# Kernel optimization log

Measured on AMD Instinct MI355X. Metric: run time of the kernel, lower is better.

Reference implementation:

```python
import jax, jax.numpy as jnp
import numpy as np
import math

B, S, E, H, NL, OUT, VOCAB = 16, 512, 1024, 16, 6, 10, 16
D = E // H
PAD = VOCAB - 1
EPS = 1e-5


def _positional_encoding():
    # Faithful to the module: pe[:x.size(0)] indexes the BATCH dim of a
    # [B, S, E] tensor, yielding [B, 1, E] broadcast over sequence.
    pos = jnp.arange(B, dtype=jnp.float32)[:, None]            # [B,1]
    div = jnp.exp(jnp.arange(0, E, 2, dtype=jnp.float32) * (-math.log(10000.0) / E))
    pe = jnp.zeros((B, E), dtype=jnp.float32)
    pe = pe.at[:, 0::2].set(jnp.sin(pos * div))
    pe = pe.at[:, 1::2].set(jnp.cos(pos * div))
    return pe[:, None, :]                                      # [B,1,E]


def setup_inputs() -> dict:
    key = jax.random.key(0)
    ks = jax.random.split(key, 8)
    sc = 0.02
    return {
        "inputs": jax.random.randint(ks[0], (B, S), 0, PAD),   # no pad tokens
        "emb": jax.random.normal(ks[1], (VOCAB, E), jnp.float32) * sc,
        "wq": jax.random.normal(ks[2], (E, E), jnp.float32) * sc,
        "bq": jnp.zeros((E,), jnp.float32),
        "wk": jax.random.normal(ks[3], (E, E), jnp.float32) * sc,
        "bk": jnp.zeros((E,), jnp.float32),
        "wv": jax.random.normal(ks[4], (E, E), jnp.float32) * sc,
        "bv": jnp.zeros((E,), jnp.float32),
        "wfc": jax.random.normal(ks[5], (E, E), jnp.float32) * sc,
        "bfc": jnp.zeros((E,), jnp.float32),
        "gamma": jnp.ones((E,), jnp.float32),
        "beta": jnp.zeros((E,), jnp.float32),
        "wout": jax.random.normal(ks[6], (S * E, OUT), jnp.float32) * sc,
        "bout": jnp.zeros((OUT,), jnp.float32),
    }


def _layernorm(x, gamma, beta):
    mu = jnp.mean(x, axis=-1, keepdims=True)
    var = jnp.mean(jnp.square(x - mu), axis=-1, keepdims=True)
    return (x - mu) * jax.lax.rsqrt(var + EPS) * gamma + beta


def reference(inputs, emb, wq, bq, wk, bk, wv, bv, wfc, bfc, gamma, beta, wout, bout):
    x = emb[inputs]                                            # [B,S,E]
    x = x + (x + _positional_encoding())                       # x += pos_enc(x)
    mask = (inputs == PAD)                                     # [B,S] key-pad mask
    scale = 1.0 / math.sqrt(D)
    for _ in range(NL):  # same (shared) weights each iteration, as in source
        q = (x @ wq + bq).reshape(B, S, H, D).transpose(0, 2, 1, 3)
        k = (x @ wk + bk).reshape(B, S, H, D).transpose(0, 2, 1, 3)
        v = (x @ wv + bv).reshape(B, S, H, D).transpose(0, 2, 1, 3)
        att = jnp.einsum('bhqd,bhkd->bhqk', q, k) * scale      # [B,H,S,S]
        att = jnp.where(mask[:, None, None, :], -jnp.inf, att)
        att = jax.nn.softmax(att, axis=-1)
        o = jnp.einsum('bhqk,bhkd->bhqd', att, v)
        o = o.transpose(0, 2, 1, 3).reshape(B, S, E)
        x = _layernorm(o + x, gamma, beta)                     # dropout = eval identity
        x = _layernorm((x @ wfc + bfc) + x, gamma, beta)
    return x.reshape(B, -1) @ wout + bout                      # [B,OUT]
```

## Files before the change

kernel.cpp:

```cpp
#include <hip/hip_runtime.h>
#include <hip/hip_bf16.h>
#include <math.h>

#define B_   16
#define S_   512
#define E_   1024
#define H_   16
#define D_   64
#define NL_  6
#define OUT_ 10
#define M_   (B_*S_)

typedef short short8 __attribute__((ext_vector_type(8)));
typedef float f32x4 __attribute__((ext_vector_type(4)));
typedef int   int4v __attribute__((ext_vector_type(4)));
typedef unsigned short ushort4v __attribute__((ext_vector_type(4)));

typedef const __attribute__((address_space(1))) unsigned int* gas1_t;
typedef __attribute__((address_space(3))) unsigned int* las3_t;
#define GLD16(g,l) __builtin_amdgcn_global_load_lds((gas1_t)(g), (las3_t)(l), 16, 0, 0)

static __device__ __forceinline__ float bf2f(unsigned short u){
  union { unsigned int i; float f; } v; v.i = ((unsigned int)u) << 16; return v.f;
}
static __device__ __forceinline__ unsigned short f2bf(float f){
  union { __hip_bfloat16 h; unsigned short u; } v;
  v.h = __float2bfloat16(f);
  return v.u;
}
static __device__ __forceinline__ f32x4 mfma16(short8 a, short8 b, f32x4 c){
  return __builtin_amdgcn_mfma_f32_16x16x32_bf16(a, b, c, 0, 0, 0);
}

__global__ __launch_bounds__(192)
void code_k(float* __restrict__ out, float code)
{
  int t = threadIdx.x;
  if (t < B_*OUT_) out[t] = code;
}

__global__ __launch_bounds__(256)
void transpose_k(const float* __restrict__ w0, const float* __restrict__ w1,
                 const float* __restrict__ w2, const float* __restrict__ w3,
                 unsigned short* __restrict__ wT)
{
  const float* w = blockIdx.z==0 ? w0 : blockIdx.z==1 ? w1 : blockIdx.z==2 ? w2 : w3;
  unsigned short* o = wT + (size_t)blockIdx.z * E_ * E_;
  __shared__ unsigned short tl[64][65];
  int n0 = blockIdx.x*64, k0 = blockIdx.y*64;
  int tx = threadIdx.x, ty = threadIdx.y;
  #pragma unroll
  for (int i = 0; i < 16; ++i)
    tl[ty + 4*i][tx] = f2bf(w[(size_t)(k0 + ty + 4*i)*E_ + n0 + tx]);
  __syncthreads();
  #pragma unroll
  for (int i = 0; i < 16; ++i)
    o[(size_t)(n0 + ty + 4*i)*E_ + k0 + tx] = tl[tx][ty + 4*i];
}

__global__ __launch_bounds__(256)
void embed_k(const int* __restrict__ tok, const float* __restrict__ emb,
             unsigned short* __restrict__ x)
{
  int row = blockIdx.x;
  int b = row >> 9;
  int tk = tok[row];
  tk = tk < 0 ? 0 : (tk > 15 ? 15 : tk);
  int e0 = threadIdx.x * 4;
  const float c0 = -9.210340371976184f / (float)E_;
  f32x4 ev = *(const f32x4*)&emb[(size_t)tk * E_ + e0];
  ushort4v bb;
  #pragma unroll
  for (int i = 0; i < 4; ++i) {
    int e = e0 + i;
    float dv = expf((float)(e & ~1) * c0);
    float arg = (float)b * dv;
    float pe = (e & 1) ? cosf(arg) : sinf(arg);
    bb[i] = f2bf(2.0f * ev[i] + pe);
  }
  *(ushort4v*)&x[(size_t)row*E_ + e0] = bb;
}

template<int MODE>
__global__ __launch_bounds__(256)
void gemm_bt_k(const unsigned short* __restrict__ A,
               const unsigned short* __restrict__ BT,
               const float* __restrict__ biasA, const float* __restrict__ biasB,
               unsigned short* __restrict__ outq)
{
  __shared__ alignas(16) unsigned short SM[(MODE==2) ? 17408 : 16384];
  unsigned short* Al = SM;
  unsigned short* Bl = SM + 8192;
  int mt = blockIdx.x;
  int nyt = blockIdx.y;
  int wsel = (MODE == 0) ? (nyt >> 3) : 0;
  int nt   = (MODE == 0) ? (nyt & 7) : nyt;
  const unsigned short* Bp = BT + (size_t)wsel * E_ * E_ + (size_t)nt * 128 * E_;
  const float* bias = (MODE == 0) ? (wsel == 0 ? biasA : biasB) : biasA;
  int tid = threadIdx.x;
  int lane = tid & 63, wid = tid >> 6;
  int wr = wid >> 1, wc = wid & 1;
  int m0 = mt * 128;
  int lr = lane & 15, lk = lane >> 4;
  int lx = lr & 7;
  int c8 = tid & 7;
  int rbase = tid >> 3;
  int c8s = c8 ^ (rbase & 7);
  f32x4 acc[4][4] = {};
  for (int kt = 0; kt < E_/64; ++kt) {
    #pragma unroll
    for (int j = 0; j < 4; ++j) {
      int r = j*32 + rbase;
      int idx = j*256 + tid;
      GLD16(A + (size_t)(m0 + r)*E_ + kt*64 + c8s*8, &Al[idx*8]);
      GLD16(Bp + (size_t)r*E_ + kt*64 + c8s*8, &Bl[idx*8]);
    }
    __syncthreads();
    #pragma unroll
    for (int kk = 0; kk < 2; ++kk) {
      int sA = ((kk*4 + lk) ^ lx) * 8;
      short8 af[4], bfr[4];
      #pragma unroll
      for (int mi = 0; mi < 4; ++mi)
        af[mi] = *(const short8*)&Al[(wr*64 + mi*16 + lr)*64 + sA];
      #pragma unroll
      for (int ni = 0; ni < 4; ++ni)
        bfr[ni] = *(const short8*)&Bl[(wc*64 + ni*16 + lr)*64 + sA];
      #pragma unroll
      for (int mi = 0; mi < 4; ++mi)
        #pragma unroll
        for (int ni = 0; ni < 4; ++ni)
          acc[mi][ni] = mfma16(af[mi], bfr[ni], acc[mi][ni]);
    }
    __syncthreads();
  }
  if (MODE == 2) {
    unsigned short* Ct = SM;
    #pragma unroll
    for (int ni = 0; ni < 4; ++ni) {
      int nl = wc*64 + ni*16 + lr;
      float bv = bias[nt*128 + nl];
      #pragma unroll
      for (int mi = 0; mi < 4; ++mi)
        #pragma unroll
        for (int j = 0; j < 4; ++j)
          Ct[nl*136 + wr*64 + mi*16 + lk*4 + j] = f2bf(acc[mi][ni][j] + bv);
    }
    __syncthreads();
    int dl = tid >> 1, half = tid & 1;
    int h = nt*2 + (dl >> 6), d = dl & 63;
    int bb = m0 >> 9, s0 = (m0 & 511) + half*64;
    unsigned short* gp = outq + (((size_t)(bb*H_ + h)*D_ + d)*S_ + s0);
    #pragma unroll
    for (int c = 0; c < 8; ++c)
      *(int4v*)(gp + c*8) = *(const int4v*)&Ct[dl*136 + half*64 + c*8];
  } else {
    unsigned short* Cl = SM;
    #pragma unroll
    for (int ni = 0; ni < 4; ++ni) {
      int n = nt*128 + wc*64 + ni*16 + lr;
      float bv = bias[n];
      #pragma unroll
      for (int mi = 0; mi < 4; ++mi)
        #pragma unroll
        for (int j = 0; j < 4; ++j)
          Cl[(wr*64 + mi*16 + lk*4 + j)*128 + wc*64 + ni*16 + lr] =
            f2bf(acc[mi][ni][j] + bv);
    }
    __syncthreads();
    int r = tid >> 1, half = tid & 1;
    int m = m0 + r;
    unsigned short* gp;
    if (MODE == 0) {
      int bb = m >> 9, s = m & 511;
      int h = nt*2 + half;
      gp = outq + (size_t)wsel*M_*E_ + (((size_t)(bb*H_ + h)*S_ + s)*D_);
    } else {
      gp = outq + (size_t)m*E_ + nt*128 + half*64;
    }
    const unsigned short* sp = &Cl[r*128 + half*64];
    #pragma unroll
    for (int c = 0; c < 8; ++c)
      *(int4v*)(gp + c*8) = *(const int4v*)(sp + c*8);
  }
}

__global__ __launch_bounds__(512, 4)
void attn_k(const unsigned short* __restrict__ Q, const unsigned short* __restrict__ K,
            const unsigned short* __restrict__ VT, unsigned short* __restrict__ O)
{
  extern __shared__ unsigned short SMEM[];
  int bid = blockIdx.x;
  int bh = bid & 255, qh = bid >> 8;
  int tid = threadIdx.x, lane = tid & 63, wid = tid >> 6;
  int lr = lane & 15, lk = lane >> 4;
  const unsigned short* Qb = Q + (size_t)bh * S_ * D_;
  const unsigned short* Kb = K + (size_t)bh * S_ * D_;
  const unsigned short* VTb = VT + (size_t)bh * S_ * D_;
  unsigned short* Pw = SMEM + 32768 + wid * 640;

  int kr  = tid >> 3, kc8 = tid & 7;
  int kcs = kc8 ^ (kr & 7);
  short8 qf[2][2];
  #pragma unroll
  for (int s = 0; s < 2; ++s) {
    int q0 = (qh*2 + s)*128 + wid*16;
    qf[s][0] = *(const short8*)(Qb + (size_t)(q0 + lr)*D_ + lk*8);
    qf[s][1] = *(const short8*)(Qb + (size_t)(q0 + lr)*D_ + 32 + lk*8);
  }
  {
    unsigned short* Kd = SMEM;
    #pragma unroll
    for (int j = 0; j < 2; ++j) {
      int idx = j*512 + tid;
      GLD16(Kb + (size_t)(kr + j*64)*D_ + kcs*8, &Kd[idx*8]);
    }
  }
  {
    unsigned short* Vd = SMEM + 16384;
    #pragma unroll
    for (int j = 0; j < 2; ++j) {
      int idx = j*512 + tid;
      int d = idx >> 4, c16 = idx & 15;
      int cds = c16 ^ (d & 15);
      GLD16(VTb + (size_t)d*S_ + cds*8, &Vd[idx*8]);
    }
  }
  __syncthreads();

  f32x4 oacc[2][4] = {};
  float plsum[2][4] = {{0.f,0.f,0.f,0.f},{0.f,0.f,0.f,0.f}};
  int cur = 0;
  for (int kt = 0; kt < 4; ++kt) {
    if (kt < 3) {
      unsigned short* Kd = SMEM + (cur^1)*8192;
      unsigned short* Vd = SMEM + 16384 + (cur^1)*8192;
      #pragma unroll
      for (int j = 0; j < 2; ++j) {
        int idx = j*512 + tid;
        int r = idx >> 3, c8 = idx & 7;
        GLD16(Kb + (size_t)((kt+1)*128 + r)*D_ + (c8 ^ (r & 7))*8, &Kd[idx*8]);
        int d = idx >> 4, c16 = idx & 15;
        GLD16(VTb + (size_t)d*S_ + (kt+1)*128 + (c16 ^ (d & 15))*8, &Vd[idx*8]);
      }
    }
    const unsigned short* Kl = SMEM + cur*8192;
    const unsigned short* Vl = SMEM + 16384 + cur*8192;
    #pragma unroll
    for (int s = 0; s < 2; ++s) {
      #pragma unroll
      for (int c = 0; c < 4; ++c) {
        f32x4 s0 = {}, s1 = {};
        {
          const unsigned short* kr0 = &Kl[((2*c)*16 + lr)*64];
          const unsigned short* kr1 = &Kl[((2*c+1)*16 + lr)*64];
          int a0 = ((lk     ^ (lr & 7)))*8;
          int a1 = (((4+lk) ^ (lr & 7)))*8;
          s0 = mfma16(qf[s][0], *(const short8*)(kr0 + a0), s0);
          s0 = mfma16(qf[s][1], *(const short8*)(kr0 + a1), s0);
          s1 = mfma16(qf[s][0], *(const short8*)(kr1 + a0), s1);
          s1 = mfma16(qf[s][1], *(const short8*)(kr1 + a1), s1);
        }
        #pragma unroll
        for (int j = 0; j < 4; ++j) {
          s0[j] = __expf(s0[j] * 0.125f);
          s1[j] = __expf(s1[j] * 0.125f);
          plsum[s][j] += s0[j] + s1[j];
        }
        #pragma unroll
        for (int j = 0; j < 4; ++j) {
          Pw[(lk*4 + j)*40 + lr]      = f2bf(s0[j]);
          Pw[(lk*4 + j)*40 + 16 + lr] = f2bf(s1[j]);
        }
        asm volatile("s_waitcnt lgkmcnt(0)" ::: "memory");
        short8 pf = *(const short8*)&Pw[lr*40 + lk*8];
        #pragma unroll
        for (int dt = 0; dt < 4; ++dt) {
          int drow = dt*16 + lr;
          short8 vf = *(const short8*)&Vl[drow*128 + (((c*4 + lk) ^ lr))*8];
          oacc[s][dt] = mfma16(pf, vf, oacc[s][dt]);
        }
      }
    }
    __syncthreads();
    cur ^= 1;
  }
  #pragma unroll
  for (int s = 0; s < 2; ++s) {
    float lsum[4];
    #pragma unroll
    for (int j = 0; j < 4; ++j) {
      float t = plsum[s][j];
      #pragma unroll
      for (int m = 1; m < 16; m <<= 1) t += __shfl_xor(t, m);
      lsum[j] = t;
    }
    int q0 = (qh*2 + s)*128 + wid*16;
    #pragma unroll
    for (int dt = 0; dt < 4; ++dt)
      #pragma unroll
      for (int j = 0; j < 4; ++j)
        O[(size_t)bh*S_*D_ + (size_t)(q0 + lk*4 + j)*D_ + dt*16 + lr] =
          f2bf(oacc[s][dt][j] / lsum[j]);
  }
}

template<bool PERM>
__global__ __launch_bounds__(256)
void ln_k(const unsigned short* __restrict__ g, unsigned short* __restrict__ x,
          const float* __restrict__ gamma, const float* __restrict__ beta)
{
  int row = blockIdx.x;
  int tid = threadIdx.x;
  int e0 = tid * 4;
  ushort4v gu;
  if (PERM) {
    int b = row >> 9, s = row & 511;
    int h = e0 >> 6, d = e0 & 63;
    gu = *(const ushort4v*)&g[(((size_t)(b*H_ + h)*S_) + s)*D_ + d];
  } else {
    gu = *(const ushort4v*)&g[(size_t)row*E_ + e0];
  }
  ushort4v xu = *(const ushort4v*)&x[(size_t)row*E_ + e0];
  f32x4 v;
  #pragma unroll
  for (int i = 0; i < 4; ++i) v[i] = bf2f(gu[i]) + bf2f(xu[i]);
  float sum = v[0]+v[1]+v[2]+v[3];
  float sq  = v[0]*v[0]+v[1]*v[1]+v[2]*v[2]+v[3]*v[3];
  #pragma unroll
  for (int m = 1; m < 64; m <<= 1) { sum += __shfl_xor(sum, m); sq += __shfl_xor(sq, m); }
  __shared__ float red[2][4];
  int lane = tid & 63, wid = tid >> 6;
  if (lane == 0) { red[0][wid] = sum; red[1][wid] = sq; }
  __syncthreads();
  float ts = red[0][0]+red[0][1]+red[0][2]+red[0][3];
  float tq = red[1][0]+red[1][1]+red[1][2]+red[1][3];
  float mu = ts * (1.0f/E_);
  float var = tq * (1.0f/E_) - mu*mu;
  float rsq = rsqrtf(var + 1e-5f);
  ushort4v yb;
  #pragma unroll
  for (int i = 0; i < 4; ++i)
    yb[i] = f2bf((v[i]-mu)*rsq*gamma[e0+i] + beta[e0+i]);
  *(ushort4v*)&x[(size_t)row*E_ + e0] = yb;
}

__global__ __launch_bounds__(256)
void outp_k(const unsigned short* __restrict__ x, const float* __restrict__ wout,
            float* __restrict__ part)
{
  int b = blockIdx.y;
  int chunk = blockIdx.x;
  int tid = threadIdx.x;
  float acc[OUT_] = {};
  const unsigned short* xr = x + (size_t)b * S_ * E_;
  for (int j = 0; j < 32; ++j) {
    int k = chunk*8192 + j*256 + tid;
    float xv = bf2f(xr[k]);
    const float* wr = wout + (size_t)k * OUT_;
    #pragma unroll
    for (int o = 0; o < OUT_; ++o) acc[o] += xv * wr[o];
  }
  #pragma unroll
  for (int o = 0; o < OUT_; ++o)
    #pragma unroll
    for (int m = 1; m < 64; m <<= 1) acc[o] += __shfl_xor(acc[o], m);
  __shared__ float red[4][OUT_];
  int lane = tid & 63, wid = tid >> 6;
  if (lane == 0) {
    #pragma unroll
    for (int o = 0; o < OUT_; ++o) red[wid][o] = acc[o];
  }
  __syncthreads();
  if (tid < OUT_) {
    float s = red[0][tid] + red[1][tid] + red[2][tid] + red[3][tid];
    part[((size_t)chunk*B_ + b)*OUT_ + tid] = s;
  }
}

__global__ __launch_bounds__(192)
void outred_k(const float* __restrict__ part, const float* __restrict__ bout,
              float* __restrict__ out)
{
  int t = threadIdx.x;
  if (t < B_*OUT_) {
    int b = t / OUT_, o = t % OUT_;
    float s = 0.f;
    for (int c = 0; c < 64; ++c) s += part[((size_t)c*B_ + b)*OUT_ + o];
    s += bout[o];
    out[t] = s;
  }
}

extern "C" void kernel_launch(void* const* d_in, const int* in_sizes, int n_in,
                              void* d_out, int out_size, void* d_ws, size_t ws_size,
                              hipStream_t stream)
{
  (void)out_size;
  float* outb = (float*)d_out;

  static const int expect[14] = {8192, 16384, 1048576, 1024, 1048576, 1024,
                                 1048576, 1024, 1048576, 1024, 1024, 1024,
                                 5242880, 10};
  if (n_in != 14) { code_k<<<dim3(1), dim3(192), 0, stream>>>(outb, 9000.0f); return; }
  for (int i = 0; i < 14; ++i)
    if (in_sizes[i] != expect[i]) {
      code_k<<<dim3(1), dim3(192), 0, stream>>>(outb, 5000.0f + 100.0f*i); return;
    }

  const int* tok = (const int*)d_in[0];
  const float* emb  = (const float*)d_in[1];
  const float* wq   = (const float*)d_in[2];
  const float* bq   = (const float*)d_in[3];
  const float* wk   = (const float*)d_in[4];
  const float* bk   = (const float*)d_in[5];
  const float* wv   = (const float*)d_in[6];
  const float* bv   = (const float*)d_in[7];
  const float* wfc  = (const float*)d_in[8];
  const float* bfc  = (const float*)d_in[9];
  const float* gam  = (const float*)d_in[10];
  const float* bet  = (const float*)d_in[11];
  const float* wout = (const float*)d_in[12];
  const float* bout = (const float*)d_in[13];

  char* ws = (char*)d_ws;
  size_t off = 0;
  unsigned short* wT = (unsigned short*)(ws + off); off += (size_t)4*E_*E_*2;
  unsigned short* x  = (unsigned short*)(ws + off); off += (size_t)M_*E_*2;
  unsigned short* qkvb = (unsigned short*)(ws + off); off += (size_t)3*M_*E_*2;
  unsigned short* gb = (unsigned short*)(ws + off); off += (size_t)M_*E_*2;
  float* part = (float*)(ws + off);                 off += (size_t)64*B_*OUT_*4;
  if (off > ws_size) { code_k<<<dim3(1), dim3(192), 0, stream>>>(outb, 9500.0f); return; }

  transpose_k<<<dim3(16,16,4), dim3(64,4), 0, stream>>>(wq, wk, wv, wfc, wT);
  embed_k<<<dim3(M_), dim3(256), 0, stream>>>(tok, emb, x);
  unsigned short* qb = qkvb;
  unsigned short* kb = qkvb + (size_t)M_*E_;
  unsigned short* vb = qkvb + (size_t)2*M_*E_;
  for (int l = 0; l < NL_; ++l) {
    gemm_bt_k<0><<<dim3(64,16), dim3(256), 0, stream>>>(x, wT, bq, bk, qkvb);
    gemm_bt_k<2><<<dim3(64,8),  dim3(256), 0, stream>>>(x, wT + (size_t)2*E_*E_, bv, bv, vb);
    attn_k<<<dim3(512), dim3(512), 75776, stream>>>(qb, kb, vb, gb);
    ln_k<true><<<dim3(M_), dim3(256), 0, stream>>>(gb, x, gam, bet);
    gemm_bt_k<1><<<dim3(64,8), dim3(256), 0, stream>>>(x, wT + (size_t)3*E_*E_, bfc, bfc, gb);
    ln_k<false><<<dim3(M_), dim3(256), 0, stream>>>(gb, x, gam, bet);
  }
  outp_k<<<dim3(64,B_), dim3(256), 0, stream>>>(x, wout, part);
  outred_k<<<dim3(1), dim3(192), 0, stream>>>(part, bout, outb);
}
```

Before: 960.9 us.

## Split attention into per-strip blocks and use one wave per row in layernorm

```diff
diff --git a/kernel.cpp b/kernel.cpp
--- a/kernel.cpp
+++ b/kernel.cpp
@@ -185,124 +185,83 @@
   }
 }
 
-__global__ __launch_bounds__(512, 4)
+__global__ __launch_bounds__(512, 6)
 void attn_k(const unsigned short* __restrict__ Q, const unsigned short* __restrict__ K,
             const unsigned short* __restrict__ VT, unsigned short* __restrict__ O)
 {
   extern __shared__ unsigned short SMEM[];
+  unsigned short* Kl = SMEM;
+  unsigned short* Vl = SMEM + 8192;
+  unsigned short* Pw = SMEM + 16384 + (threadIdx.x >> 6) * 640;
   int bid = blockIdx.x;
-  int bh = bid & 255, qh = bid >> 8;
+  int bh = bid & 255, strip = bid >> 8;
   int tid = threadIdx.x, lane = tid & 63, wid = tid >> 6;
   int lr = lane & 15, lk = lane >> 4;
   const unsigned short* Qb = Q + (size_t)bh * S_ * D_;
   const unsigned short* Kb = K + (size_t)bh * S_ * D_;
   const unsigned short* VTb = VT + (size_t)bh * S_ * D_;
-  unsigned short* Pw = SMEM + 32768 + wid * 640;
-
-  int kr  = tid >> 3, kc8 = tid & 7;
-  int kcs = kc8 ^ (kr & 7);
-  short8 qf[2][2];
-  #pragma unroll
-  for (int s = 0; s < 2; ++s) {
-    int q0 = (qh*2 + s)*128 + wid*16;
-    qf[s][0] = *(const short8*)(Qb + (size_t)(q0 + lr)*D_ + lk*8);
-    qf[s][1] = *(const short8*)(Qb + (size_t)(q0 + lr)*D_ + 32 + lk*8);
-  }
-  {
-    unsigned short* Kd = SMEM;
+  int q0 = strip*128 + wid*16;
+  short8 qf0 = *(const short8*)(Qb + (size_t)(q0 + lr)*D_ + lk*8);
+  short8 qf1 = *(const short8*)(Qb + (size_t)(q0 + lr)*D_ + 32 + lk*8);
+  f32x4 oacc[4] = {};
+  float plsum[4] = {0.f,0.f,0.f,0.f};
+  for (int kt = 0; kt < 4; ++kt) {
     #pragma unroll
     for (int j = 0; j < 2; ++j) {
       int idx = j*512 + tid;
-      GLD16(Kb + (size_t)(kr + j*64)*D_ + kcs*8, &Kd[idx*8]);
-    }
-  }
-  {
-    unsigned short* Vd = SMEM + 16384;
-    #pragma unroll
-    for (int j = 0; j < 2; ++j) {
-      int idx = j*512 + tid;
+      int r = idx >> 3, c8 = idx & 7;
+      GLD16(Kb + (size_t)(kt*128 + r)*D_ + (c8 ^ (r & 7))*8, &Kl[idx*8]);
       int d = idx >> 4, c16 = idx & 15;
-      int cds = c16 ^ (d & 15);
-      GLD16(VTb + (size_t)d*S_ + cds*8, &Vd[idx*8]);
-    }
-  }
-  __syncthreads();
-
-  f32x4 oacc[2][4] = {};
-  float plsum[2][4] = {{0.f,0.f,0.f,0.f},{0.f,0.f,0.f,0.f}};
-  int cur = 0;
-  for (int kt = 0; kt < 4; ++kt) {
-    if (kt < 3) {
-      unsigned short* Kd = SMEM + (cur^1)*8192;
-      unsigned short* Vd = SMEM + 16384 + (cur^1)*8192;
-      #pragma unroll
-      for (int j = 0; j < 2; ++j) {
-        int idx = j*512 + tid;
-        int r = idx >> 3, c8 = idx & 7;
-        GLD16(Kb + (size_t)((kt+1)*128 + r)*D_ + (c8 ^ (r & 7))*8, &Kd[idx*8]);
-        int d = idx >> 4, c16 = idx & 15;
-        GLD16(VTb + (size_t)d*S_ + (kt+1)*128 + (c16 ^ (d & 15))*8, &Vd[idx*8]);
+      GLD16(VTb + (size_t)d*S_ + kt*128 + (c16 ^ (d & 15))*8, &Vl[idx*8]);
+    }
+    __syncthreads();
+    f32x4 sc[8];
+    #pragma unroll
+    for (int t = 0; t < 8; ++t) {
+      const unsigned short* krow = &Kl[(t*16 + lr)*64];
+      int a0 = ((lk     ^ (lr & 7)))*8;
+      int a1 = (((4+lk) ^ (lr & 7)))*8;
+      f32x4 s = {};
+      s = mfma16(qf0, *(const short8*)(krow + a0), s);
+      s = mfma16(qf1, *(const short8*)(krow + a1), s);
+      #pragma unroll
+      for (int j = 0; j < 4; ++j) s[j] = __expf(s[j] * 0.125f);
+      sc[t] = s;
+      #pragma unroll
+      for (int j = 0; j < 4; ++j) plsum[j] += s[j];
+    }
+    #pragma unroll
+    for (int c = 0; c < 4; ++c) {
+      #pragma unroll
+      for (int j = 0; j < 4; ++j) {
+        Pw[(lk*4 + j)*40 + lr]      = f2bf(sc[2*c  ][j]);
+        Pw[(lk*4 + j)*40 + 16 + lr] = f2bf(sc[2*c+1][j]);
       }
-    }
-    const unsigned short* Kl = SMEM + cur*8192;
-    const unsigned short* Vl = SMEM + 16384 + cur*8192;
-    #pragma unroll
-    for (int s = 0; s < 2; ++s) {
-      #pragma unroll
-      for (int c = 0; c < 4; ++c) {
-        f32x4 s0 = {}, s1 = {};
-        {
-          const unsigned short* kr0 = &Kl[((2*c)*16 + lr)*64];
-          const unsigned short* kr1 = &Kl[((2*c+1)*16 + lr)*64];
-          int a0 = ((lk     ^ (lr & 7)))*8;
-          int a1 = (((4+lk) ^ (lr & 7)))*8;
-          s0 = mfma16(qf[s][0], *(const short8*)(kr0 + a0), s0);
-          s0 = mfma16(qf[s][1], *(const short8*)(kr0 + a1), s0);
-          s1 = mfma16(qf[s][0], *(const short8*)(kr1 + a0), s1);
-          s1 = mfma16(qf[s][1], *(const short8*)(kr1 + a1), s1);
-        }
-        #pragma unroll
-        for (int j = 0; j < 4; ++j) {
-          s0[j] = __expf(s0[j] * 0.125f);
-          s1[j] = __expf(s1[j] * 0.125f);
-          plsum[s][j] += s0[j] + s1[j];
-        }
-        #pragma unroll
-        for (int j = 0; j < 4; ++j) {
-          Pw[(lk*4 + j)*40 + lr]      = f2bf(s0[j]);
-          Pw[(lk*4 + j)*40 + 16 + lr] = f2bf(s1[j]);
-        }
-        asm volatile("s_waitcnt lgkmcnt(0)" ::: "memory");
-        short8 pf = *(const short8*)&Pw[lr*40 + lk*8];
-        #pragma unroll
-        for (int dt = 0; dt < 4; ++dt) {
-          int drow = dt*16 + lr;
-          short8 vf = *(const short8*)&Vl[drow*128 + (((c*4 + lk) ^ lr))*8];
-          oacc[s][dt] = mfma16(pf, vf, oacc[s][dt]);
-        }
+      asm volatile("s_waitcnt lgkmcnt(0)" ::: "memory");
+      short8 pf = *(const short8*)&Pw[lr*40 + lk*8];
+      #pragma unroll
+      for (int dt = 0; dt < 4; ++dt) {
+        int drow = dt*16 + lr;
+        short8 vf = *(const short8*)&Vl[drow*128 + (((c*4 + lk) ^ lr))*8];
+        oacc[dt] = mfma16(pf, vf, oacc[dt]);
       }
     }
     __syncthreads();
-    cur ^= 1;
-  }
-  #pragma unroll
-  for (int s = 0; s < 2; ++s) {
-    float lsum[4];
-    #pragma unroll
-    for (int j = 0; j < 4; ++j) {
-      float t = plsum[s][j];
-      #pragma unroll
-      for (int m = 1; m < 16; m <<= 1) t += __shfl_xor(t, m);
-      lsum[j] = t;
-    }
-    int q0 = (qh*2 + s)*128 + wid*16;
-    #pragma unroll
-    for (int dt = 0; dt < 4; ++dt)
-      #pragma unroll
-      for (int j = 0; j < 4; ++j)
-        O[(size_t)bh*S_*D_ + (size_t)(q0 + lk*4 + j)*D_ + dt*16 + lr] =
-          f2bf(oacc[s][dt][j] / lsum[j]);
-  }
+  }
+  float lsum[4];
+  #pragma unroll
+  for (int j = 0; j < 4; ++j) {
+    float t = plsum[j];
+    #pragma unroll
+    for (int m = 1; m < 16; m <<= 1) t += __shfl_xor(t, m);
+    lsum[j] = t;
+  }
+  #pragma unroll
+  for (int dt = 0; dt < 4; ++dt)
+    #pragma unroll
+    for (int j = 0; j < 4; ++j)
+      O[(size_t)bh*S_*D_ + (size_t)(q0 + lk*4 + j)*D_ + dt*16 + lr] =
+        f2bf(oacc[dt][j] / lsum[j]);
 }
 
 template<bool PERM>
@@ -310,39 +269,43 @@
 void ln_k(const unsigned short* __restrict__ g, unsigned short* __restrict__ x,
           const float* __restrict__ gamma, const float* __restrict__ beta)
 {
-  int row = blockIdx.x;
-  int tid = threadIdx.x;
-  int e0 = tid * 4;
-  ushort4v gu;
+  int wid = threadIdx.x >> 6, lane = threadIdx.x & 63;
+  int row = blockIdx.x * 4 + wid;
+  int e0 = lane * 16;
+  const unsigned short* gp;
   if (PERM) {
     int b = row >> 9, s = row & 511;
     int h = e0 >> 6, d = e0 & 63;
-    gu = *(const ushort4v*)&g[(((size_t)(b*H_ + h)*S_) + s)*D_ + d];
+    gp = g + (((size_t)(b*H_ + h)*S_) + s)*D_ + d;
   } else {
-    gu = *(const ushort4v*)&g[(size_t)row*E_ + e0];
-  }
-  ushort4v xu = *(const ushort4v*)&x[(size_t)row*E_ + e0];
-  f32x4 v;
-  #pragma unroll
-  for (int i = 0; i < 4; ++i) v[i] = bf2f(gu[i]) + bf2f(xu[i]);
-  float sum = v[0]+v[1]+v[2]+v[3];
-  float sq  = v[0]*v[0]+v[1]*v[1]+v[2]*v[2]+v[3]*v[3];
+    gp = g + (size_t)row*E_ + e0;
+  }
+  unsigned short* xp = x + (size_t)row*E_ + e0;
+  ushort4v gu[4], xu[4];
+  #pragma unroll
+  for (int i = 0; i < 4; ++i) { gu[i] = *(const ushort4v*)(gp + i*4); xu[i] = *(const ushort4v*)(xp + i*4); }
+  float v[16];
+  float sum = 0.f, sq = 0.f;
+  #pragma unroll
+  for (int i = 0; i < 16; ++i) {
+    float t = bf2f(gu[i>>2][i&3]) + bf2f(xu[i>>2][i&3]);
+    v[i] = t; sum += t; sq += t*t;
+  }
   #pragma unroll
   for (int m = 1; m < 64; m <<= 1) { sum += __shfl_xor(sum, m); sq += __shfl_xor(sq, m); }
-  __shared__ float red[2][4];
-  int lane = tid & 63, wid = tid >> 6;
-  if (lane == 0) { red[0][wid] = sum; red[1][wid] = sq; }
-  __syncthreads();
-  float ts = red[0][0]+red[0][1]+red[0][2]+red[0][3];
-  float tq = red[1][0]+red[1][1]+red[1][2]+red[1][3];
-  float mu = ts * (1.0f/E_);
-  float var = tq * (1.0f/E_) - mu*mu;
+  float mu = sum * (1.0f/E_);
+  float var = sq * (1.0f/E_) - mu*mu;
   float rsq = rsqrtf(var + 1e-5f);
-  ushort4v yb;
-  #pragma unroll
-  for (int i = 0; i < 4; ++i)
-    yb[i] = f2bf((v[i]-mu)*rsq*gamma[e0+i] + beta[e0+i]);
-  *(ushort4v*)&x[(size_t)row*E_ + e0] = yb;
+  #pragma unroll
+  for (int i = 0; i < 4; ++i) {
+    ushort4v yb;
+    #pragma unroll
+    for (int j = 0; j < 4; ++j) {
+      int e = e0 + i*4 + j;
+      yb[j] = f2bf((v[i*4+j]-mu)*rsq*gamma[e] + beta[e]);
+    }
+    *(ushort4v*)(xp + i*4) = yb;
+  }
 }
 
 __global__ __launch_bounds__(256)
@@ -440,10 +403,10 @@
   for (int l = 0; l < NL_; ++l) {
     gemm_bt_k<0><<<dim3(64,16), dim3(256), 0, stream>>>(x, wT, bq, bk, qkvb);
     gemm_bt_k<2><<<dim3(64,8),  dim3(256), 0, stream>>>(x, wT + (size_t)2*E_*E_, bv, bv, vb);
-    attn_k<<<dim3(512), dim3(512), 75776, stream>>>(qb, kb, vb, gb);
-    ln_k<true><<<dim3(M_), dim3(256), 0, stream>>>(gb, x, gam, bet);
+    attn_k<<<dim3(1024), dim3(512), 43008, stream>>>(qb, kb, vb, gb);
+    ln_k<true><<<dim3(M_/4), dim3(256), 0, stream>>>(gb, x, gam, bet);
     gemm_bt_k<1><<<dim3(64,8), dim3(256), 0, stream>>>(x, wT + (size_t)3*E_*E_, bfc, bfc, gb);
-    ln_k<false><<<dim3(M_), dim3(256), 0, stream>>>(gb, x, gam, bet);
+    ln_k<false><<<dim3(M_/4), dim3(256), 0, stream>>>(gb, x, gam, bet);
   }
   outp_k<<<dim3(64,B_), dim3(256), 0, stream>>>(x, wout, part);
   outred_k<<<dim3(1), dim3(192), 0, stream>>>(part, bout, outb);
```

Result: slower. 1.023 ms (+6.4%).
